# Performance work log

Measured on AMD Instinct MI355X. Metric: run time of the kernel, lower is better.

The kernel has to match this reference:

```python
import jax, jax.numpy as jnp
import numpy as np

B, N = 4, 8192
NPOINT, NSAMPLE = 2048, 16
IN_PLANES, OUT_PLANES = 64, 128
EPS = 1e-5


def farthest_point_sample(xyz, npoint):
    # xyz: (B, N, 3) -> (B, npoint) int32 indices. Deterministic start at index 0
    # (torch version uses a random start; fixed start keeps the reference reproducible).
    Bb, Nn, _ = xyz.shape

    def step(carry, _):
        distance, farthest = carry                                   # (B,N), (B,)
        centroid = jnp.take_along_axis(xyz, farthest[:, None, None], axis=1)  # (B,1,3)
        dist = jnp.sum((xyz - centroid) ** 2, axis=-1)               # (B,N)
        distance = jnp.minimum(distance, dist)
        new_farthest = jnp.argmax(distance, axis=-1).astype(jnp.int32)
        return (distance, new_farthest), farthest

    init = (jnp.full((Bb, Nn), 1e10, xyz.dtype), jnp.zeros((Bb,), jnp.int32))
    _, cents = jax.lax.scan(step, init, None, length=npoint)         # (npoint, B)
    return cents.T                                                   # (B, npoint)


def setup_inputs() -> dict:
    key = jax.random.key(0)
    k1, k2, k3 = jax.random.split(key, 3)
    px = jax.random.normal(k1, (B, N, IN_PLANES), jnp.float32)
    xyz = jax.random.uniform(k2, (B, N, 3), jnp.float32)
    # Linear(3+in_planes -> out_planes), stored as (in, out)
    W = jax.random.normal(k3, (3 + IN_PLANES, OUT_PLANES), jnp.float32) * 0.1
    b = jnp.zeros((OUT_PLANES,), jnp.float32)
    gamma = jnp.ones((OUT_PLANES,), jnp.float32)
    beta = jnp.zeros((OUT_PLANES,), jnp.float32)
    return {"px": px, "xyz": xyz, "W": W, "b": b, "gamma": gamma, "beta": beta}


def reference(px, xyz, W, b, gamma, beta):
    Bb, Nn, C = px.shape
    cent_idx = farthest_point_sample(xyz, NPOINT)                    # (B, npoint)
    new_xyz = jnp.take_along_axis(xyz, cent_idx[:, :, None], axis=1) # (B, npoint, 3)

    # squared pairwise distances, clamped at 0 (matches square_distance)
    dists = (jnp.sum(new_xyz ** 2, -1)[..., None]
             + jnp.sum(xyz ** 2, -1)[:, None, :]
             - 2.0 * jnp.einsum('bmc,bnc->bmn', new_xyz, xyz))       # (B, npoint, N)
    dists = jnp.maximum(dists, 0.0)

    # KNN: top_k on negated dists == argsort()[:, :, :nsample] up to ties
    _, idx = jax.lax.top_k(-dists, NSAMPLE)                          # (B, npoint, nsample)

    gather = jax.vmap(lambda pts, i: pts[i])                         # per-batch fancy gather
    grouped_xyz = gather(xyz, idx)                                   # (B, npoint, nsample, 3)
    grouped_px = gather(px, idx)                                     # (B, npoint, nsample, C)
    grouped_xyz_norm = grouped_xyz - new_xyz[:, :, None, :]
    grouped = jnp.concatenate([grouped_px, grouped_xyz_norm], axis=-1)

    # Linear -> BatchNorm1d (training-mode batch stats, biased var) -> ReLU
    h = grouped.reshape(-1, C + 3) @ W + b                           # (B*npoint*nsample, out)
    mu = jnp.mean(h, axis=0)
    var = jnp.var(h, axis=0)
    h = (h - mu) / jnp.sqrt(var + EPS) * gamma + beta
    h = jax.nn.relu(h)

    new_px = jnp.max(h.reshape(Bb, NPOINT, NSAMPLE, -1), axis=2)     # (B, npoint, out)
    return new_px, new_xyz
```

## Files before the change

### kernel.cpp

```cpp
#include <hip/hip_runtime.h>
#include <math.h>

#define Bc 4
#define Nc 8192
#define NPOINTc 2048
#define NSAMPLEc 16
#define CINc 64
#define COUTc 128
#define FDIMc 67
#define NBUCK 128
#define EPSc 1e-5f

__global__ void sq_norm_kernel(const float* __restrict__ xyz, float* __restrict__ sn) {
    int i = blockIdx.x * blockDim.x + threadIdx.x;
    if (i < Bc * Nc) {
        float x = xyz[i * 3], y = xyz[i * 3 + 1], z = xyz[i * 3 + 2];
        sn[i] = __fadd_rn(__fadd_rn(__fmul_rn(x, x), __fmul_rn(y, y)), __fmul_rn(z, z));
    }
}

template <int CTRL>
__device__ __forceinline__ void amax_dpp(float& bd, int& bi) {
    const int od_i = __builtin_amdgcn_update_dpp(__float_as_int(bd), __float_as_int(bd),
                                                 CTRL, 0xF, 0xF, false);
    const int oi   = __builtin_amdgcn_update_dpp(bi, bi, CTRL, 0xF, 0xF, false);
    const float od = __int_as_float(od_i);
    if (od > bd || (od == bd && oi < bi)) { bd = od; bi = oi; }
}

__global__ __launch_bounds__(512) void fps_kernel(const float* __restrict__ xyz,
                                                  int* __restrict__ cent,
                                                  float* __restrict__ newxyz) {
    const int b = blockIdx.x;
    const float* base = xyz + (size_t)b * Nc * 3;
    const int t = threadIdx.x;
    const int lane = t & 63, wid = t >> 6;

    __shared__ float P[Nc * 3];
    __shared__ float pd[2][8];
    __shared__ int   pi[2][8];

    for (int e = t; e < Nc * 3; e += 512) P[e] = base[e];

    float X[16], Y[16], Z[16], D[16];
#pragma unroll
    for (int k = 0; k < 16; ++k) {
        const int n = t + (k << 9);
        X[k] = base[n * 3 + 0];
        Y[k] = base[n * 3 + 1];
        Z[k] = base[n * 3 + 2];
        D[k] = 1e10f;
    }
    if (t == 0) {
        cent[b * NPOINTc] = 0;
        float* o = newxyz + (size_t)b * NPOINTc * 3;
        o[0] = base[0]; o[1] = base[1]; o[2] = base[2];
    }
    __syncthreads();

    float cx = P[0], cy = P[1], cz = P[2];

    for (int it = 1; it < NPOINTc; ++it) {
#pragma unroll
        for (int k = 0; k < 16; ++k) {
            const float dx = __fsub_rn(X[k], cx);
            const float dy = __fsub_rn(Y[k], cy);
            const float dz = __fsub_rn(Z[k], cz);
            const float d2 = __fadd_rn(__fadd_rn(__fmul_rn(dx, dx), __fmul_rn(dy, dy)),
                                       __fmul_rn(dz, dz));
            if (d2 < D[k]) D[k] = d2;
        }
        float a0[8]; int x0[8];
#pragma unroll
        for (int k = 0; k < 8; ++k) {
            const bool g = D[2 * k + 1] > D[2 * k];
            a0[k] = g ? D[2 * k + 1] : D[2 * k];
            x0[k] = t + ((g ? (2 * k + 1) : (2 * k)) << 9);
        }
        float a1[4]; int x1[4];
#pragma unroll
        for (int k = 0; k < 4; ++k) {
            const bool g = a0[2 * k + 1] > a0[2 * k];
            a1[k] = g ? a0[2 * k + 1] : a0[2 * k];
            x1[k] = g ? x0[2 * k + 1] : x0[2 * k];
        }
        float a2[2]; int x2[2];
#pragma unroll
        for (int k = 0; k < 2; ++k) {
            const bool g = a1[2 * k + 1] > a1[2 * k];
            a2[k] = g ? a1[2 * k + 1] : a1[2 * k];
            x2[k] = g ? x1[2 * k + 1] : x1[2 * k];
        }
        float bd = (a2[1] > a2[0]) ? a2[1] : a2[0];
        int   bi = (a2[1] > a2[0]) ? x2[1] : x2[0];

        amax_dpp<0x111>(bd, bi);
        amax_dpp<0x112>(bd, bi);
        amax_dpp<0x114>(bd, bi);
        amax_dpp<0x118>(bd, bi);
        amax_dpp<0x142>(bd, bi);
        amax_dpp<0x143>(bd, bi);

        const int par = it & 1;
        if (lane == 63) { pd[par][wid] = bd; pi[par][wid] = bi; }
        __syncthreads();

        float d8 = (lane < 8) ? pd[par][lane] : -INFINITY;
        int   i8 = (lane < 8) ? pi[par][lane] : 0x7fffffff;
        amax_dpp<0x111>(d8, i8);
        amax_dpp<0x112>(d8, i8);
        amax_dpp<0x114>(d8, i8);
        const int riv = __builtin_amdgcn_readlane(i8, 7);

        cx = P[riv * 3 + 0]; cy = P[riv * 3 + 1]; cz = P[riv * 3 + 2];

        if (t == 0) {
            cent[b * NPOINTc + it] = riv;
            float* o = newxyz + ((size_t)b * NPOINTc + it) * 3;
            o[0] = cx; o[1] = cy; o[2] = cz;
        }
    }
}

__global__ __launch_bounds__(64) void knn_kernel(const float* __restrict__ xyz,
                                                 const float* __restrict__ sn,
                                                 const int* __restrict__ cent,
                                                 int* __restrict__ knn) {
    const int g = blockIdx.x;
    const int b = g >> 11;
    const int lane = threadIdx.x;
    const float* base = xyz + (size_t)b * Nc * 3;
    const float* snb = sn + (size_t)b * Nc;

    const int cm = cent[g];
    const float mx = base[cm * 3 + 0];
    const float my = base[cm * 3 + 1];
    const float mz = base[cm * 3 + 2];
    const float s1 = snb[cm];

    float dls[16];
    int   ils[16];
#pragma unroll
    for (int j = 0; j < 16; ++j) { dls[j] = INFINITY; ils[j] = -1; }

    for (int jj = 0; jj < Nc / 64; ++jj) {
        const int n = lane + (jj << 6);
        const float x = base[n * 3 + 0];
        const float y = base[n * 3 + 1];
        const float z = base[n * 3 + 2];
        const float dot = fmaf(z, mz, fmaf(y, my, __fmul_rn(x, mx)));
        float d = __fadd_rn(__fadd_rn(__fmul_rn(-2.0f, dot), s1), snb[n]);
        d = fmaxf(d, 0.0f);
        if (d < dls[15]) {
            float cd = d; int ci = n;
#pragma unroll
            for (int j = 0; j < 16; ++j) {
                const bool less = cd < dls[j];
                const float td = less ? dls[j] : cd;
                const int   ti = less ? ils[j] : ci;
                dls[j] = less ? cd : dls[j];
                ils[j] = less ? ci : ils[j];
                cd = td; ci = ti;
            }
        }
    }

    __shared__ float ld[64][16];
    __shared__ int   li[64][16];
#pragma unroll
    for (int j = 0; j < 16; ++j) { ld[lane][j] = dls[j]; li[lane][j] = ils[j]; }

    int ptr = 0;
    int* out = knn + (size_t)g * NSAMPLEc;
    for (int r = 0; r < NSAMPLEc; ++r) {
        const float hd = ld[lane][ptr];
        const int   hi = li[lane][ptr];
        float vd = hd; int vi = hi;
#pragma unroll
        for (int off = 32; off > 0; off >>= 1) {
            const float od = __shfl_xor(vd, off, 64);
            const int   oi = __shfl_xor(vi, off, 64);
            if (od < vd || (od == vd && oi < vi)) { vd = od; vi = oi; }
        }
        if (hd == vd && hi == vi) ptr++;
        if (lane == r) out[r] = vi;
    }
}

__device__ __forceinline__ void stage_featT(
        const float* __restrict__ px, const float* __restrict__ xyz,
        const float* __restrict__ newxyz, const int* __restrict__ knn,
        int g, int b, int t, float (*featT)[20], int* nidx, float* ctr) {
    if (t < 16) nidx[t] = knn[(size_t)g * NSAMPLEc + t];
    if (t < 3)  ctr[t] = newxyz[(size_t)g * 3 + t];
    __syncthreads();
    for (int e = t; e < 16 * FDIMc; e += 128) {
        const int s = e / FDIMc, i = e % FDIMc;
        float v;
        if (i < CINc) v = px[((size_t)b * Nc + nidx[s]) * CINc + i];
        else          v = __fsub_rn(xyz[((size_t)b * Nc + nidx[s]) * 3 + (i - CINc)], ctr[i - CINc]);
        featT[i][s] = v;
    }
    __syncthreads();
}

__global__ __launch_bounds__(128) void gemm_stats_kernel(
        const float* __restrict__ px, const float* __restrict__ xyz,
        const float* __restrict__ newxyz, const int* __restrict__ knn,
        const float* __restrict__ W, const float* __restrict__ bias,
        float* __restrict__ bsum, float* __restrict__ bsq) {
    const int g = blockIdx.x;
    const int b = g >> 11;
    const int t = threadIdx.x;

    __shared__ __align__(16) float featT[FDIMc][20];
    __shared__ int nidx[16];
    __shared__ float ctr[3];
    stage_featT(px, xyz, newxyz, knn, g, b, t, featT, nidx, ctr);

    float acc[16];
    const float bc = bias[t];
#pragma unroll
    for (int r = 0; r < 16; ++r) acc[r] = bc;

    for (int i = 0; i < FDIMc; ++i) {
        const float w = W[i * COUTc + t];
        const float4* fr = (const float4*)featT[i];
        const float4 f0 = fr[0], f1 = fr[1], f2 = fr[2], f3 = fr[3];
        acc[0]  = fmaf(f0.x, w, acc[0]);  acc[1]  = fmaf(f0.y, w, acc[1]);
        acc[2]  = fmaf(f0.z, w, acc[2]);  acc[3]  = fmaf(f0.w, w, acc[3]);
        acc[4]  = fmaf(f1.x, w, acc[4]);  acc[5]  = fmaf(f1.y, w, acc[5]);
        acc[6]  = fmaf(f1.z, w, acc[6]);  acc[7]  = fmaf(f1.w, w, acc[7]);
        acc[8]  = fmaf(f2.x, w, acc[8]);  acc[9]  = fmaf(f2.y, w, acc[9]);
        acc[10] = fmaf(f2.z, w, acc[10]); acc[11] = fmaf(f2.w, w, acc[11]);
        acc[12] = fmaf(f3.x, w, acc[12]); acc[13] = fmaf(f3.y, w, acc[13]);
        acc[14] = fmaf(f3.z, w, acc[14]); acc[15] = fmaf(f3.w, w, acc[15]);
    }
    float s = 0.f, q = 0.f;
#pragma unroll
    for (int r = 0; r < 16; ++r) { s += acc[r]; q += acc[r] * acc[r]; }
    atomicAdd(&bsum[(g & (NBUCK - 1)) * COUTc + t], s);
    atomicAdd(&bsq [(g & (NBUCK - 1)) * COUTc + t], q);
}

__global__ void stats_finalize_kernel(const float* __restrict__ bsum,
                                      const float* __restrict__ bsq,
                                      const float* __restrict__ gamma,
                                      const float* __restrict__ beta,
                                      float* __restrict__ scsh) {
    const int c = threadIdx.x;
    float S = 0.f, Q = 0.f;
    for (int k = 0; k < NBUCK; ++k) { S += bsum[k * COUTc + c]; Q += bsq[k * COUTc + c]; }
    const float cnt = (float)(Bc * NPOINTc * NSAMPLEc);
    const float mu = S / cnt;
    const float var = Q / cnt - mu * mu;
    const float sc = gamma[c] / sqrtf(var + EPSc);
    scsh[c] = sc;
    scsh[COUTc + c] = beta[c] - mu * sc;
}

__global__ __launch_bounds__(128) void gemm_out_kernel(
        const float* __restrict__ px, const float* __restrict__ xyz,
        const float* __restrict__ newxyz, const int* __restrict__ knn,
        const float* __restrict__ W, const float* __restrict__ bias,
        const float* __restrict__ scsh, float* __restrict__ out) {
    const int g = blockIdx.x;
    const int b = g >> 11;
    const int t = threadIdx.x;

    __shared__ __align__(16) float featT[FDIMc][20];
    __shared__ int nidx[16];
    __shared__ float ctr[3];
    stage_featT(px, xyz, newxyz, knn, g, b, t, featT, nidx, ctr);

    float acc[16];
    const float bc = bias[t];
#pragma unroll
    for (int r = 0; r < 16; ++r) acc[r] = bc;

    for (int i = 0; i < FDIMc; ++i) {
        const float w = W[i * COUTc + t];
        const float4* fr = (const float4*)featT[i];
        const float4 f0 = fr[0], f1 = fr[1], f2 = fr[2], f3 = fr[3];
        acc[0]  = fmaf(f0.x, w, acc[0]);  acc[1]  = fmaf(f0.y, w, acc[1]);
        acc[2]  = fmaf(f0.z, w, acc[2]);  acc[3]  = fmaf(f0.w, w, acc[3]);
        acc[4]  = fmaf(f1.x, w, acc[4]);  acc[5]  = fmaf(f1.y, w, acc[5]);
        acc[6]  = fmaf(f1.z, w, acc[6]);  acc[7]  = fmaf(f1.w, w, acc[7]);
        acc[8]  = fmaf(f2.x, w, acc[8]);  acc[9]  = fmaf(f2.y, w, acc[9]);
        acc[10] = fmaf(f2.z, w, acc[10]); acc[11] = fmaf(f2.w, w, acc[11]);
        acc[12] = fmaf(f3.x, w, acc[12]); acc[13] = fmaf(f3.y, w, acc[13]);
        acc[14] = fmaf(f3.z, w, acc[14]); acc[15] = fmaf(f3.w, w, acc[15]);
    }

    const float sc = scsh[t], sh = scsh[COUTc + t];
    float m = -INFINITY;
#pragma unroll
    for (int r = 0; r < 16; ++r) {
        const float v = fmaxf(fmaf(acc[r], sc, sh), 0.0f);
        m = fmaxf(m, v);
    }
    out[(size_t)g * COUTc + t] = m;
}

extern "C" void kernel_launch(void* const* d_in, const int* in_sizes, int n_in,
                              void* d_out, int out_size, void* d_ws, size_t ws_size,
                              hipStream_t stream) {
    const float* px    = (const float*)d_in[0];
    const float* xyz   = (const float*)d_in[1];
    const float* W     = (const float*)d_in[2];
    const float* bias  = (const float*)d_in[3];
    const float* gamma = (const float*)d_in[4];
    const float* beta  = (const float*)d_in[5];

    float* out_px = (float*)d_out;
    float* out_nx = out_px + (size_t)Bc * NPOINTc * COUTc;

    char* w = (char*)d_ws;
    int*   cent = (int*)w;    w += (size_t)Bc * NPOINTc * 4;
    float* sn   = (float*)w;  w += (size_t)Bc * Nc * 4;
    int*   knn  = (int*)w;    w += (size_t)Bc * NPOINTc * NSAMPLEc * 4;
    float* bsum = (float*)w;  w += (size_t)NBUCK * COUTc * 4;
    float* bsq  = (float*)w;  w += (size_t)NBUCK * COUTc * 4;
    float* scsh = (float*)w;  w += 2 * COUTc * 4;

    hipMemsetAsync(bsum, 0, (size_t)NBUCK * COUTc * 4 * 2, stream);

    sq_norm_kernel<<<(Bc * Nc + 255) / 256, 256, 0, stream>>>(xyz, sn);
    fps_kernel<<<Bc, 512, 0, stream>>>(xyz, cent, out_nx);
    knn_kernel<<<Bc * NPOINTc, 64, 0, stream>>>(xyz, sn, cent, knn);
    gemm_stats_kernel<<<Bc * NPOINTc, 128, 0, stream>>>(px, xyz, out_nx, knn, W, bias, bsum, bsq);
    stats_finalize_kernel<<<1, 128, 0, stream>>>(bsum, bsq, gamma, beta, scsh);
    gemm_out_kernel<<<Bc * NPOINTc, 128, 0, stream>>>(px, xyz, out_nx, knn, W, bias, scsh, out_px);
}
```

Measured before the change: 3.288 ms.

## Store per-group max/min to skip second GEMM pass; shrink FPS block

The GEMM-stats kernel now also records each group's per-channel max and min of the pre-norm activations. A light finalize kernel then applies the BN affine to max or min, picking by the sign of the scale, followed by ReLU. This avoids re-gathering features and recomputing the GEMM in a second pass, at the cost of writing and reading two B*npoint*128 float buffers, and it falls back to the old path if the workspace is too small. FPS moves from 512 to 256 threads with 32 points per thread, which cuts the cross-wave reduction and barrier work but doubles per-thread register and compute serialization.

```diff
diff --git a/kernel.cpp b/kernel.cpp
--- a/kernel.cpp
+++ b/kernel.cpp
@@ -28,24 +28,24 @@
     if (od > bd || (od == bd && oi < bi)) { bd = od; bi = oi; }
 }
 
-__global__ __launch_bounds__(512) void fps_kernel(const float* __restrict__ xyz,
-                                                  int* __restrict__ cent,
-                                                  float* __restrict__ newxyz) {
+__global__ __launch_bounds__(256, 1) void fps_kernel(const float* __restrict__ xyz,
+                                                     int* __restrict__ cent,
+                                                     float* __restrict__ newxyz) {
     const int b = blockIdx.x;
     const float* base = xyz + (size_t)b * Nc * 3;
     const int t = threadIdx.x;
     const int lane = t & 63, wid = t >> 6;
 
     __shared__ float P[Nc * 3];
-    __shared__ float pd[2][8];
-    __shared__ int   pi[2][8];
-
-    for (int e = t; e < Nc * 3; e += 512) P[e] = base[e];
-
-    float X[16], Y[16], Z[16], D[16];
-#pragma unroll
-    for (int k = 0; k < 16; ++k) {
-        const int n = t + (k << 9);
+    __shared__ float pd[2][4];
+    __shared__ int   pi[2][4];
+
+    for (int e = t; e < Nc * 3; e += 256) P[e] = base[e];
+
+    float X[32], Y[32], Z[32], D[32];
+#pragma unroll
+    for (int k = 0; k < 32; ++k) {
+        const int n = t + (k << 8);
         X[k] = base[n * 3 + 0];
         Y[k] = base[n * 3 + 1];
         Z[k] = base[n * 3 + 2];
@@ -62,37 +62,44 @@
 
     for (int it = 1; it < NPOINTc; ++it) {
 #pragma unroll
-        for (int k = 0; k < 16; ++k) {
+        for (int k = 0; k < 32; ++k) {
             const float dx = __fsub_rn(X[k], cx);
             const float dy = __fsub_rn(Y[k], cy);
             const float dz = __fsub_rn(Z[k], cz);
             const float d2 = __fadd_rn(__fadd_rn(__fmul_rn(dx, dx), __fmul_rn(dy, dy)),
                                        __fmul_rn(dz, dz));
-            if (d2 < D[k]) D[k] = d2;
-        }
-        float a0[8]; int x0[8];
-#pragma unroll
-        for (int k = 0; k < 8; ++k) {
+            D[k] = fminf(D[k], d2);
+        }
+        float a0[16]; int x0[16];
+#pragma unroll
+        for (int k = 0; k < 16; ++k) {
             const bool g = D[2 * k + 1] > D[2 * k];
             a0[k] = g ? D[2 * k + 1] : D[2 * k];
-            x0[k] = t + ((g ? (2 * k + 1) : (2 * k)) << 9);
-        }
-        float a1[4]; int x1[4];
-#pragma unroll
-        for (int k = 0; k < 4; ++k) {
+            x0[k] = t + ((g ? (2 * k + 1) : (2 * k)) << 8);
+        }
+        float a1[8]; int x1[8];
+#pragma unroll
+        for (int k = 0; k < 8; ++k) {
             const bool g = a0[2 * k + 1] > a0[2 * k];
             a1[k] = g ? a0[2 * k + 1] : a0[2 * k];
             x1[k] = g ? x0[2 * k + 1] : x0[2 * k];
         }
-        float a2[2]; int x2[2];
-#pragma unroll
-        for (int k = 0; k < 2; ++k) {
+        float a2[4]; int x2[4];
+#pragma unroll
+        for (int k = 0; k < 4; ++k) {
             const bool g = a1[2 * k + 1] > a1[2 * k];
             a2[k] = g ? a1[2 * k + 1] : a1[2 * k];
             x2[k] = g ? x1[2 * k + 1] : x1[2 * k];
         }
-        float bd = (a2[1] > a2[0]) ? a2[1] : a2[0];
-        int   bi = (a2[1] > a2[0]) ? x2[1] : x2[0];
+        float a3[2]; int x3[2];
+#pragma unroll
+        for (int k = 0; k < 2; ++k) {
+            const bool g = a2[2 * k + 1] > a2[2 * k];
+            a3[k] = g ? a2[2 * k + 1] : a2[2 * k];
+            x3[k] = g ? x2[2 * k + 1] : x2[2 * k];
+        }
+        float bd = (a3[1] > a3[0]) ? a3[1] : a3[0];
+        int   bi = (a3[1] > a3[0]) ? x3[1] : x3[0];
 
         amax_dpp<0x111>(bd, bi);
         amax_dpp<0x112>(bd, bi);
@@ -105,12 +112,11 @@
         if (lane == 63) { pd[par][wid] = bd; pi[par][wid] = bi; }
         __syncthreads();
 
-        float d8 = (lane < 8) ? pd[par][lane] : -INFINITY;
-        int   i8 = (lane < 8) ? pi[par][lane] : 0x7fffffff;
-        amax_dpp<0x111>(d8, i8);
-        amax_dpp<0x112>(d8, i8);
-        amax_dpp<0x114>(d8, i8);
-        const int riv = __builtin_amdgcn_readlane(i8, 7);
+        float d4 = (lane < 4) ? pd[par][lane] : -INFINITY;
+        int   i4 = (lane < 4) ? pi[par][lane] : 0x7fffffff;
+        amax_dpp<0x111>(d4, i4);
+        amax_dpp<0x112>(d4, i4);
+        const int riv = __builtin_amdgcn_readlane(i4, 3);
 
         cx = P[riv * 3 + 0]; cy = P[riv * 3 + 1]; cz = P[riv * 3 + 2];
 
@@ -204,25 +210,10 @@
     __syncthreads();
 }
 
-__global__ __launch_bounds__(128) void gemm_stats_kernel(
-        const float* __restrict__ px, const float* __restrict__ xyz,
-        const float* __restrict__ newxyz, const int* __restrict__ knn,
-        const float* __restrict__ W, const float* __restrict__ bias,
-        float* __restrict__ bsum, float* __restrict__ bsq) {
-    const int g = blockIdx.x;
-    const int b = g >> 11;
-    const int t = threadIdx.x;
-
-    __shared__ __align__(16) float featT[FDIMc][20];
-    __shared__ int nidx[16];
-    __shared__ float ctr[3];
-    stage_featT(px, xyz, newxyz, knn, g, b, t, featT, nidx, ctr);
-
-    float acc[16];
-    const float bc = bias[t];
+__device__ __forceinline__ void gemm_body(const float (*featT)[20], const float* __restrict__ W,
+                                          float bc, int t, float* acc) {
 #pragma unroll
     for (int r = 0; r < 16; ++r) acc[r] = bc;
-
     for (int i = 0; i < FDIMc; ++i) {
         const float w = W[i * COUTc + t];
         const float4* fr = (const float4*)featT[i];
@@ -236,11 +227,34 @@
         acc[12] = fmaf(f3.x, w, acc[12]); acc[13] = fmaf(f3.y, w, acc[13]);
         acc[14] = fmaf(f3.z, w, acc[14]); acc[15] = fmaf(f3.w, w, acc[15]);
     }
-    float s = 0.f, q = 0.f;
+}
+
+__global__ __launch_bounds__(128) void gemm_stats_kernel(
+        const float* __restrict__ px, const float* __restrict__ xyz,
+        const float* __restrict__ newxyz, const int* __restrict__ knn,
+        const float* __restrict__ W, const float* __restrict__ bias,
+        float* __restrict__ bsum, float* __restrict__ bsq,
+        float* __restrict__ hmax, float* __restrict__ hmin) {
+    const int g = blockIdx.x;
+    const int b = g >> 11;
+    const int t = threadIdx.x;
+
+    __shared__ __align__(16) float featT[FDIMc][20];
+    __shared__ int nidx[16];
+    __shared__ float ctr[3];
+    stage_featT(px, xyz, newxyz, knn, g, b, t, featT, nidx, ctr);
+
+    float acc[16];
+    gemm_body(featT, W, bias[t], t, acc);
+
+    float s = 0.f, q = 0.f, mx = acc[0], mn = acc[0];
 #pragma unroll
     for (int r = 0; r < 16; ++r) { s += acc[r]; q += acc[r] * acc[r]; }
+#pragma unroll
+    for (int r = 1; r < 16; ++r) { mx = fmaxf(mx, acc[r]); mn = fminf(mn, acc[r]); }
     atomicAdd(&bsum[(g & (NBUCK - 1)) * COUTc + t], s);
     atomicAdd(&bsq [(g & (NBUCK - 1)) * COUTc + t], q);
+    if (hmax) { hmax[(size_t)g * COUTc + t] = mx; hmin[(size_t)g * COUTc + t] = mn; }
 }
 
 __global__ void stats_finalize_kernel(const float* __restrict__ bsum,
@@ -259,6 +273,16 @@
     scsh[COUTc + c] = beta[c] - mu * sc;
 }
 
+__global__ __launch_bounds__(256) void finalize_out_kernel(
+        const float* __restrict__ hmax, const float* __restrict__ hmin,
+        const float* __restrict__ scsh, float* __restrict__ out) {
+    const int i = blockIdx.x * 256 + threadIdx.x;
+    const int c = i & (COUTc - 1);
+    const float sc = scsh[c], sh = scsh[COUTc + c];
+    const float sel = (sc > 0.f) ? hmax[i] : hmin[i];
+    out[i] = fmaxf(fmaf(sel, sc, sh), 0.0f);
+}
+
 __global__ __launch_bounds__(128) void gemm_out_kernel(
         const float* __restrict__ px, const float* __restrict__ xyz,
         const float* __restrict__ newxyz, const int* __restrict__ knn,
@@ -274,23 +298,7 @@
     stage_featT(px, xyz, newxyz, knn, g, b, t, featT, nidx, ctr);
 
     float acc[16];
-    const float bc = bias[t];
-#pragma unroll
-    for (int r = 0; r < 16; ++r) acc[r] = bc;
-
-    for (int i = 0; i < FDIMc; ++i) {
-        const float w = W[i * COUTc + t];
-        const float4* fr = (const float4*)featT[i];
-        const float4 f0 = fr[0], f1 = fr[1], f2 = fr[2], f3 = fr[3];
-        acc[0]  = fmaf(f0.x, w, acc[0]);  acc[1]  = fmaf(f0.y, w, acc[1]);
-        acc[2]  = fmaf(f0.z, w, acc[2]);  acc[3]  = fmaf(f0.w, w, acc[3]);
-        acc[4]  = fmaf(f1.x, w, acc[4]);  acc[5]  = fmaf(f1.y, w, acc[5]);
-        acc[6]  = fmaf(f1.z, w, acc[6]);  acc[7]  = fmaf(f1.w, w, acc[7]);
-        acc[8]  = fmaf(f2.x, w, acc[8]);  acc[9]  = fmaf(f2.y, w, acc[9]);
-        acc[10] = fmaf(f2.z, w, acc[10]); acc[11] = fmaf(f2.w, w, acc[11]);
-        acc[12] = fmaf(f3.x, w, acc[12]); acc[13] = fmaf(f3.y, w, acc[13]);
-        acc[14] = fmaf(f3.z, w, acc[14]); acc[15] = fmaf(f3.w, w, acc[15]);
-    }
+    gemm_body(featT, W, bias[t], t, acc);
 
     const float sc = scsh[t], sh = scsh[COUTc + t];
     float m = -INFINITY;
@@ -315,20 +323,31 @@
     float* out_px = (float*)d_out;
     float* out_nx = out_px + (size_t)Bc * NPOINTc * COUTc;
 
-    char* w = (char*)d_ws;
+    char* w0 = (char*)d_ws;
+    char* w = w0;
     int*   cent = (int*)w;    w += (size_t)Bc * NPOINTc * 4;
     float* sn   = (float*)w;  w += (size_t)Bc * Nc * 4;
     int*   knn  = (int*)w;    w += (size_t)Bc * NPOINTc * NSAMPLEc * 4;
     float* bsum = (float*)w;  w += (size_t)NBUCK * COUTc * 4;
     float* bsq  = (float*)w;  w += (size_t)NBUCK * COUTc * 4;
     float* scsh = (float*)w;  w += 2 * COUTc * 4;
+    float* hmax = (float*)w;  w += (size_t)Bc * NPOINTc * COUTc * 4;
+    float* hmin = (float*)w;  w += (size_t)Bc * NPOINTc * COUTc * 4;
+    const bool fused = ((size_t)(w - w0) <= ws_size);
 
     hipMemsetAsync(bsum, 0, (size_t)NBUCK * COUTc * 4 * 2, stream);
 
     sq_norm_kernel<<<(Bc * Nc + 255) / 256, 256, 0, stream>>>(xyz, sn);
-    fps_kernel<<<Bc, 512, 0, stream>>>(xyz, cent, out_nx);
+    fps_kernel<<<Bc, 256, 0, stream>>>(xyz, cent, out_nx);
     knn_kernel<<<Bc * NPOINTc, 64, 0, stream>>>(xyz, sn, cent, knn);
-    gemm_stats_kernel<<<Bc * NPOINTc, 128, 0, stream>>>(px, xyz, out_nx, knn, W, bias, bsum, bsq);
+    gemm_stats_kernel<<<Bc * NPOINTc, 128, 0, stream>>>(px, xyz, out_nx, knn, W, bias,
+                                                        bsum, bsq,
+                                                        fused ? hmax : nullptr,
+                                                        fused ? hmin : nullptr);
     stats_finalize_kernel<<<1, 128, 0, stream>>>(bsum, bsq, gamma, beta, scsh);
-    gemm_out_kernel<<<Bc * NPOINTc, 128, 0, stream>>>(px, xyz, out_nx, knn, W, bias, scsh, out_px);
-}
+    if (fused) {
+        finalize_out_kernel<<<(Bc * NPOINTc * COUTc) / 256, 256, 0, stream>>>(hmax, hmin, scsh, out_px);
+    } else {
+        gemm_out_kernel<<<Bc * NPOINTc, 128, 0, stream>>>(px, xyz, out_nx, knn, W, bias, scsh, out_px);
+    }
+}
```

After: 3.958 ms. 1.2x slower.
